# Performance work log

Measured on AMD Instinct MI355X. Metric: run time of the kernel, lower is better.

## Reference

```python
import jax, jax.numpy as jnp
import numpy as np

N = 100_000      # nodes
E = 1_600_000    # edges (avg degree 16)
C_IN, C_H, C_OUT = 32, 64, 64
G = 64           # graphs in batch


def setup_inputs() -> dict:
    key = jax.random.key(0)
    ks = jax.random.split(key, 10)
    x = jax.random.normal(ks[0], (N, C_IN), jnp.float32)
    edge_index = jax.random.randint(ks[1], (2, E), 0, N, dtype=jnp.int64)
    edge_weight = jax.random.uniform(ks[2], (E,), jnp.float32)
    batch = jnp.sort(jax.random.randint(ks[3], (N,), 0, G, dtype=jnp.int64))
    def lin(k, fan_in, fan_out):
        return jax.random.normal(k, (fan_in, fan_out), jnp.float32) / np.float32(np.sqrt(fan_in))
    W1 = lin(ks[4], C_IN, C_H)
    W2 = lin(ks[5], C_H, C_H)
    W3 = lin(ks[6], C_H, C_OUT)
    b1 = jnp.zeros((C_H,), jnp.float32)
    b2 = jnp.zeros((C_H,), jnp.float32)
    b3 = jnp.zeros((C_OUT,), jnp.float32)
    return {"x": x, "edge_weight": edge_weight, "W1": W1, "b1": b1,
            "W2": W2, "b2": b2, "W3": W3, "b3": b3,
            "edge_index": edge_index, "batch": batch}


def _gcn_norm(edge_index, edge_weight, n):
    # PyG GCNConv default: add self-loops (weight 1), symmetric D^-1/2 A D^-1/2 norm.
    loop = jnp.arange(n, dtype=edge_index.dtype)
    src = jnp.concatenate([edge_index[0], loop])
    dst = jnp.concatenate([edge_index[1], loop])
    ew = jnp.concatenate([edge_weight, jnp.ones((n,), edge_weight.dtype)])
    deg = jax.ops.segment_sum(ew, dst, num_segments=n)
    dis = jnp.where(deg > 0, jax.lax.rsqrt(deg), jnp.float32(0))
    norm = dis[src] * ew * dis[dst]
    return src, dst, norm


def _gcn_layer(h, W, b, src, dst, norm, n):
    h = h @ W                                 # [N, out]
    msg = h[src] * norm[:, None]              # gather + scale  [E+N, out]
    agg = jax.ops.segment_sum(msg, dst, num_segments=n)
    return agg + b


def reference(x, edge_weight, W1, b1, W2, b2, W3, b3, edge_index, batch):
    n = x.shape[0]
    src, dst, norm = _gcn_norm(edge_index, edge_weight, n)  # shared across layers
    h = jax.nn.silu(_gcn_layer(x, W1, b1, src, dst, norm, n))
    # Dropout(0.1) is identity in eval mode
    h = jax.nn.silu(_gcn_layer(h, W2, b2, src, dst, norm, n))
    h = jax.nn.silu(_gcn_layer(h, W3, b3, src, dst, norm, n))
    # global_mean_pool over graphs
    sums = jax.ops.segment_sum(h, batch, num_segments=G)
    counts = jax.ops.segment_sum(jnp.ones((n,), h.dtype), batch, num_segments=G)
    return sums / jnp.maximum(counts, 1)[:, None]
```

## Files before the change

kernel.cpp:

```cpp
#include <hip/hip_runtime.h>
#include <hip/hip_fp16.h>
#include <math.h>


#define NB   256
#define PBLK 1024
#define FIXP_SCALE 1048576.0f
#define FIXP_MASK  ((1ULL << 40) - 1)

__device__ __forceinline__ int lower_bound_i(const int* __restrict__ a, int n, int v) {
    int lo = 0, hi = n;
    while (lo < hi) {
        int m = (lo + hi) >> 1;
        if (a[m] < v) lo = m + 1; else hi = m;
    }
    return lo;
}

__global__ __launch_bounds__(256) void k_bhist(const int* __restrict__ dst,
                                               int* __restrict__ hcnt, int e) {
    __shared__ int hist[NB];
    int tid = threadIdx.x, blk = blockIdx.x;
    hist[tid] = 0;
    __syncthreads();
    int chunk = (e + PBLK - 1) / PBLK;
    int lo = blk * chunk, hi = min(e, lo + chunk);
    for (int i = lo + tid; i < hi; i += 256)
        atomicAdd(&hist[dst[i] >> 9], 1);
    __syncthreads();
    hcnt[tid * PBLK + blk] = hist[tid];
}

__global__ __launch_bounds__(256) void k_bscan(int* __restrict__ hcnt,
                                               int* __restrict__ btot) {
    __shared__ int s[256];
    int b = blockIdx.x, tid = threadIdx.x;
    int* row = hcnt + b * PBLK;
    int a0 = row[4 * tid], a1 = row[4 * tid + 1], a2 = row[4 * tid + 2], a3 = row[4 * tid + 3];
    int tsum = a0 + a1 + a2 + a3;
    s[tid] = tsum;
    __syncthreads();
    for (int off = 1; off < 256; off <<= 1) {
        int t = (tid >= off) ? s[tid - off] : 0;
        __syncthreads();
        s[tid] += t;
        __syncthreads();
    }
    int ex = s[tid] - tsum;
    row[4 * tid] = ex;
    row[4 * tid + 1] = ex + a0;
    row[4 * tid + 2] = ex + a0 + a1;
    row[4 * tid + 3] = ex + a0 + a1 + a2;
    if (tid == 255) btot[b] = s[255];
}

__global__ __launch_bounds__(256) void k_bbase(const int* __restrict__ btot,
                                               int* __restrict__ bbase,
                                               int* __restrict__ rowptr, int n, int e) {
    __shared__ int s[256];
    int tid = threadIdx.x;
    int v = btot[tid];
    s[tid] = v;
    __syncthreads();
    for (int off = 1; off < 256; off <<= 1) {
        int t = (tid >= off) ? s[tid - off] : 0;
        __syncthreads();
        s[tid] += t;
        __syncthreads();
    }
    bbase[tid] = s[tid] - v;
    if (tid == 255) bbase[NB] = s[255];
    if (tid == 0) rowptr[n] = e;
}

__global__ __launch_bounds__(256) void k_bpart(const int* __restrict__ src,
                                               const int* __restrict__ dst,
                                               const float* __restrict__ ew,
                                               const int* __restrict__ hcnt,
                                               const int* __restrict__ bbase,
                                               int2* __restrict__ bedge, int e) {
    __shared__ int cur[NB];
    int tid = threadIdx.x, blk = blockIdx.x;
    cur[tid] = bbase[tid] + hcnt[tid * PBLK + blk];
    __syncthreads();
    int chunk = (e + PBLK - 1) / PBLK;
    int lo = blk * chunk, hi = min(e, lo + chunk);
    for (int i = lo + tid; i < hi; i += 256) {
        int d = dst[i];
        int pos = atomicAdd(&cur[d >> 9], 1);
        bedge[pos] = make_int2(src[i] | ((d & 511) << 17), __float_as_int(ew[i]));
    }
}

__global__ __launch_bounds__(256) void k_bucket(const int2* __restrict__ bedge,
                                                const int* __restrict__ bbase,
                                                float* __restrict__ dis,
                                                int* __restrict__ rowptr,
                                                int2* __restrict__ em, int n) {
    __shared__ unsigned long long pk[512];
    __shared__ int cnt[512];
    __shared__ int scn[512];
    __shared__ float sdis[512];
    __shared__ int cur[512];
    int b = blockIdx.x, tid = threadIdx.x;
    int e0 = bbase[b], e1 = bbase[b + 1];
    pk[tid] = 0ULL; pk[tid + 256] = 0ULL;
    __syncthreads();
    for (int i = e0 + tid; i < e1; i += 256) {
        int2 v = bedge[i];
        int dlo = (v.x >> 17) & 511;
        unsigned long long p =
            (1ULL << 40) | (unsigned long long)(__int_as_float(v.y) * FIXP_SCALE);
        atomicAdd(&pk[dlo], p);
    }
    __syncthreads();
#pragma unroll
    for (int k = 0; k < 2; ++k) {
        int i = tid + k * 256;
        unsigned long long v = pk[i];
        int c = (int)(v >> 40);
        cnt[i] = c; scn[i] = c;
        sdis[i] = rsqrtf(1.0f + (float)(v & FIXP_MASK) * (1.0f / FIXP_SCALE));
    }
    __syncthreads();
    for (int off = 1; off < 512; off <<= 1) {
        int i0 = tid, i1 = tid + 256;
        int v0 = (i0 >= off) ? scn[i0 - off] : 0;
        int v1 = (i1 >= off) ? scn[i1 - off] : 0;
        __syncthreads();
        scn[i0] += v0; scn[i1] += v1;
        __syncthreads();
    }
#pragma unroll
    for (int k = 0; k < 2; ++k) {
        int i = tid + k * 256;
        int rb = e0 + scn[i] - cnt[i];
        cur[i] = rb;
        int node = (b << 9) + i;
        if (node < n) { rowptr[node] = rb; dis[node] = sdis[i]; }
    }
    __syncthreads();
    for (int i = e0 + tid; i < e1; i += 256) {
        int2 v = bedge[i];
        int dlo = (v.x >> 17) & 511;
        int pos = atomicAdd(&cur[dlo], 1);
        float w = __int_as_float(v.y) * sdis[dlo];
        em[pos] = make_int2(v.x & 0x1FFFF, __float_as_int(w));
    }
}

__global__ void k_scale(const float* __restrict__ x, const float* __restrict__ dis,
                        __half* __restrict__ hs, int total) {
    int idx = blockIdx.x * blockDim.x + threadIdx.x;
    if (idx < total) hs[idx] = __float2half(x[idx] * dis[idx >> 5]);
}

template <bool SCALE, typename OUT>
__global__ __launch_bounds__(256, 4) void k_aggmm64(const __half* __restrict__ h,
                                                    const int2* __restrict__ em,
                                                    const int* __restrict__ rowptr,
                                                    const float* __restrict__ dis,
                                                    const float* __restrict__ W,
                                                    const float* __restrict__ bias,
                                                    OUT* __restrict__ out, int n) {
    __shared__ __align__(16) float sacc[4][64];
    int lane = threadIdx.x & 63, wv = threadIdx.x >> 6;
    float w[64];
#pragma unroll
    for (int k = 0; k < 64; ++k) w[k] = W[k * 64 + lane];
    float bv = bias[lane];
    int wid = (blockIdx.x * blockDim.x + threadIdx.x) >> 6;
    int nw = (gridDim.x * blockDim.x) >> 6;
    for (int node = wid; node < n; node += nw) {
        int lo = rowptr[node], hi = rowptr[node + 1];
        int deg = hi - lo;
        float acc = dis[node] * __half2float(h[(size_t)node * 64 + lane]);
        for (int jb = 0; jb < deg; jb += 64) {
            int idx = lo + jb + lane;
            int2 me = (idx < hi) ? em[idx] : make_int2(0, 0);
            int rem = deg - jb;
#pragma unroll
            for (int g = 0; g < 4; ++g) {
                if (g * 16 < rem) {
#pragma unroll
                    for (int t = 0; t < 16; ++t) {
                        int s = __shfl(me.x, g * 16 + t, 64);
                        float ww = __int_as_float(__shfl(me.y, g * 16 + t, 64));
                        acc = fmaf(ww, __half2float(h[(size_t)s * 64 + lane]), acc);
                    }
                }
            }
        }
        sacc[wv][lane] = acc;
        float o = bv;
        const float4* s4 = (const float4*)sacc[wv];
#pragma unroll
        for (int k4 = 0; k4 < 16; ++k4) {
            float4 a4 = s4[k4];
            o = fmaf(a4.x, w[4 * k4 + 0], o);
            o = fmaf(a4.y, w[4 * k4 + 1], o);
            o = fmaf(a4.z, w[4 * k4 + 2], o);
            o = fmaf(a4.w, w[4 * k4 + 3], o);
        }
        o = o / (1.0f + __expf(-o));
        if (SCALE) o *= dis[node];
        if (sizeof(OUT) == 2) {
            ((__half*)out)[(size_t)node * 64 + lane] = __float2half(o);
        } else {
            ((float*)out)[(size_t)node * 64 + lane] = o;
        }
    }
}

__global__ __launch_bounds__(256, 4) void k_aggmm32(const __half* __restrict__ h,
                                                    const int2* __restrict__ em,
                                                    const int* __restrict__ rowptr,
                                                    const float* __restrict__ dis,
                                                    const float* __restrict__ W,
                                                    const float* __restrict__ bias,
                                                    __half* __restrict__ out, int n) {
    __shared__ __align__(16) float sacc[4][32];
    int lane = threadIdx.x & 63, wv = threadIdx.x >> 6;
    int c = lane & 31, half = lane >> 5;
    float w[32];
#pragma unroll
    for (int k = 0; k < 32; ++k) w[k] = W[k * 64 + lane];
    float bv = bias[lane];
    int wid = (blockIdx.x * blockDim.x + threadIdx.x) >> 6;
    int nw = (gridDim.x * blockDim.x) >> 6;
    for (int node = wid; node < n; node += nw) {
        int lo = rowptr[node], hi = rowptr[node + 1];
        int deg = hi - lo;
        float acc = (half == 0) ? dis[node] * __half2float(h[(size_t)node * 32 + c]) : 0.0f;
        for (int jb = 0; jb < deg; jb += 64) {
            int idx = lo + jb + lane;
            int2 me = (idx < hi) ? em[idx] : make_int2(0, 0);
            int rem = deg - jb;
#pragma unroll
            for (int g = 0; g < 4; ++g) {
                if (g * 16 < rem) {
#pragma unroll
                    for (int t = 0; t < 8; ++t) {
                        int ei = g * 16 + 2 * t + half;
                        int s = __shfl(me.x, ei, 64);
                        float ww = __int_as_float(__shfl(me.y, ei, 64));
                        acc = fmaf(ww, __half2float(h[(size_t)s * 32 + c]), acc);
                    }
                }
            }
        }
        acc += __shfl_down(acc, 32, 64);
        if (half == 0) sacc[wv][c] = acc;
        float o = bv;
        const float4* s4 = (const float4*)sacc[wv];
#pragma unroll
        for (int k4 = 0; k4 < 8; ++k4) {
            float4 a4 = s4[k4];
            o = fmaf(a4.x, w[4 * k4 + 0], o);
            o = fmaf(a4.y, w[4 * k4 + 1], o);
            o = fmaf(a4.z, w[4 * k4 + 2], o);
            o = fmaf(a4.w, w[4 * k4 + 3], o);
        }
        o = o / (1.0f + __expf(-o));
        o *= dis[node];
        out[(size_t)node * 64 + lane] = __float2half(o);
    }
}

__global__ void k_pool_partial(const float* __restrict__ h, const int* __restrict__ batch,
                               float* __restrict__ acc, int n) {
    int c = threadIdx.x & 63, r = threadIdx.x >> 6;
    int base = blockIdx.x * 128;
    int end = base + 128; if (end > n) end = n;
    float part = 0.0f;
    int cur = -1;
    for (int i = base + r; i < end; i += 4) {
        int g = batch[i];
        if (g != cur) {
            if (cur >= 0) atomicAdd(&acc[cur * 64 + c], part);
            part = 0.0f;
            cur = g;
        }
        part += h[(size_t)i * 64 + c];
    }
    if (cur >= 0) atomicAdd(&acc[cur * 64 + c], part);
}

__global__ void k_pool_final(const float* __restrict__ acc, const int* __restrict__ batch,
                             float* __restrict__ out, int n) {
    int idx = blockIdx.x * blockDim.x + threadIdx.x;
    int g = idx >> 6;
    int lo = lower_bound_i(batch, n, g);
    int hi = lower_bound_i(batch, n, g + 1);
    int cnt = hi - lo;
    out[idx] = acc[idx] / (float)(cnt > 0 ? cnt : 1);
}

extern "C" void kernel_launch(void* const* d_in, const int* in_sizes, int n_in,
                              void* d_out, int out_size, void* d_ws, size_t ws_size,
                              hipStream_t stream) {
    const float* x   = (const float*)d_in[0];
    const float* ew  = (const float*)d_in[1];
    const float* W1  = (const float*)d_in[2];
    const float* b1  = (const float*)d_in[3];
    const float* W2  = (const float*)d_in[4];
    const float* b2  = (const float*)d_in[5];
    const float* W3  = (const float*)d_in[6];
    const float* b3  = (const float*)d_in[7];
    const int*   eidx  = (const int*)d_in[8];
    const int*   batch = (const int*)d_in[9];
    float* out = (float*)d_out;

    const int E = in_sizes[1];
    const int N = in_sizes[9];
    const int G = 64;
    const int* src = eidx;
    const int* dst = eidx + E;

    char* p = (char*)d_ws;
    __half* A     = (__half*)p;                p += (size_t)N * 64 * sizeof(__half);
    __half* B     = (__half*)p;                p += (size_t)N * 64 * sizeof(__half);
    float* C      = (float*)p;                 p += (size_t)N * 64 * sizeof(float);
    float* dis    = (float*)p;                 p += (size_t)N * sizeof(float);
    int*   rowptr = (int*)p;                   p += (size_t)(N + 1) * sizeof(int);
    int*   bbase  = (int*)p;                   p += (size_t)(NB + 1) * sizeof(int);
    float* acc    = (float*)p;                 p += (size_t)G * 64 * sizeof(float);
    p = (char*)(((uintptr_t)p + 7) & ~(uintptr_t)7);
    int2*  em     = (int2*)p;

    int2* bedge = (int2*)A;
    int*  hcnt  = (int*)B;
    int*  btot  = (int*)B + NB * PBLK;

    const int BT = 256;
    const int FUSED_BLOCKS = 3125;

    k_bhist<<<PBLK, 256, 0, stream>>>(dst, hcnt, E);
    k_bscan<<<NB, 256, 0, stream>>>(hcnt, btot);
    k_bbase<<<1, 256, 0, stream>>>(btot, bbase, rowptr, N, E);
    k_bpart<<<PBLK, 256, 0, stream>>>(src, dst, ew, hcnt, bbase, bedge, E);
    k_bucket<<<NB, 256, 0, stream>>>(bedge, bbase, dis, rowptr, em, N);

    k_scale<<<(N * 32 + BT - 1) / BT, BT, 0, stream>>>(x, dis, (__half*)B, N * 32);
    k_aggmm32<<<FUSED_BLOCKS, BT, 0, stream>>>((__half*)B, em, rowptr, dis, W1, b1, A, N);

    k_aggmm64<true, __half><<<FUSED_BLOCKS, BT, 0, stream>>>(A, em, rowptr, dis, W2, b2, B, N);

    k_aggmm64<false, float><<<FUSED_BLOCKS, BT, 0, stream>>>(B, em, rowptr, dis, W3, b3, C, N);

    hipMemsetAsync(acc, 0, (size_t)G * 64 * sizeof(float), stream);
    k_pool_partial<<<(N + 127) / 128, BT, 0, stream>>>(C, batch, acc, N);
    k_pool_final<<<(G * 64) / BT, BT, 0, stream>>>(acc, batch, out, N);
}
```

Measured before the change: 386.2 us.

## Vectorize half gathers as half2 pairs and stage edge metadata in LDS

The aggregation kernels now have each lane load two channels at once as a packed half2 word. The wavefront is split into halves (64-channel) or quarters (32-channel) that handle different edges in parallel, and their partial sums are combined with shuffles. Edge indices and weights are written to per-wave shared memory and read back as int2, replacing two cross-lane shuffles per edge. The goal is more edges in flight per gather instruction and less shuffle overhead. In exchange the kernels pay for LDS traffic and extra reductions, and they rely on wave-synchronous LDS visibility with no explicit barrier.

```diff
diff --git a/kernel.cpp b/kernel.cpp
--- a/kernel.cpp
+++ b/kernel.cpp
@@ -155,6 +155,11 @@
     if (idx < total) hs[idx] = __float2half(x[idx] * dis[idx >> 5]);
 }
 
+__device__ __forceinline__ float2 cvt_pair(unsigned int u) {
+    __half2 h2 = *(__half2*)&u;
+    return __half22float2(h2);
+}
+
 template <bool SCALE, typename OUT>
 __global__ __launch_bounds__(256, 4) void k_aggmm64(const __half* __restrict__ h,
                                                     const int2* __restrict__ em,
@@ -164,7 +169,10 @@
                                                     const float* __restrict__ bias,
                                                     OUT* __restrict__ out, int n) {
     __shared__ __align__(16) float sacc[4][64];
+    __shared__ __align__(8) int2 sme[4][64];
     int lane = threadIdx.x & 63, wv = threadIdx.x >> 6;
+    int c = lane & 31, half = lane >> 5;
+    const unsigned int* h32 = (const unsigned int*)h;
     float w[64];
 #pragma unroll
     for (int k = 0; k < 64; ++k) w[k] = W[k * 64 + lane];
@@ -174,24 +182,34 @@
     for (int node = wid; node < n; node += nw) {
         int lo = rowptr[node], hi = rowptr[node + 1];
         int deg = hi - lo;
-        float acc = dis[node] * __half2float(h[(size_t)node * 64 + lane]);
+        float2 acc = make_float2(0.0f, 0.0f);
+        if (half == 0) {
+            float2 hv = cvt_pair(h32[(size_t)node * 32 + c]);
+            float di = dis[node];
+            acc.x = di * hv.x; acc.y = di * hv.y;
+        }
         for (int jb = 0; jb < deg; jb += 64) {
             int idx = lo + jb + lane;
             int2 me = (idx < hi) ? em[idx] : make_int2(0, 0);
+            sme[wv][lane] = me;
             int rem = deg - jb;
 #pragma unroll
             for (int g = 0; g < 4; ++g) {
                 if (g * 16 < rem) {
 #pragma unroll
-                    for (int t = 0; t < 16; ++t) {
-                        int s = __shfl(me.x, g * 16 + t, 64);
-                        float ww = __int_as_float(__shfl(me.y, g * 16 + t, 64));
-                        acc = fmaf(ww, __half2float(h[(size_t)s * 64 + lane]), acc);
+                    for (int t = 0; t < 8; ++t) {
+                        int2 ev = sme[wv][g * 16 + 2 * t + half];
+                        float ww = __int_as_float(ev.y);
+                        float2 hf = cvt_pair(h32[(size_t)ev.x * 32 + c]);
+                        acc.x = fmaf(ww, hf.x, acc.x);
+                        acc.y = fmaf(ww, hf.y, acc.y);
                     }
                 }
             }
         }
-        sacc[wv][lane] = acc;
+        acc.x += __shfl_down(acc.x, 32, 64);
+        acc.y += __shfl_down(acc.y, 32, 64);
+        if (half == 0) ((float2*)sacc[wv])[c] = acc;
         float o = bv;
         const float4* s4 = (const float4*)sacc[wv];
 #pragma unroll
@@ -220,8 +238,10 @@
                                                     const float* __restrict__ bias,
                                                     __half* __restrict__ out, int n) {
     __shared__ __align__(16) float sacc[4][32];
+    __shared__ __align__(8) int2 sme[4][64];
     int lane = threadIdx.x & 63, wv = threadIdx.x >> 6;
-    int c = lane & 31, half = lane >> 5;
+    int c = lane & 15, quarter = lane >> 4;
+    const unsigned int* h32 = (const unsigned int*)h;
     float w[32];
 #pragma unroll
     for (int k = 0; k < 32; ++k) w[k] = W[k * 64 + lane];
@@ -231,26 +251,36 @@
     for (int node = wid; node < n; node += nw) {
         int lo = rowptr[node], hi = rowptr[node + 1];
         int deg = hi - lo;
-        float acc = (half == 0) ? dis[node] * __half2float(h[(size_t)node * 32 + c]) : 0.0f;
+        float2 acc = make_float2(0.0f, 0.0f);
+        if (quarter == 0) {
+            float2 hv = cvt_pair(h32[(size_t)node * 16 + c]);
+            float di = dis[node];
+            acc.x = di * hv.x; acc.y = di * hv.y;
+        }
         for (int jb = 0; jb < deg; jb += 64) {
             int idx = lo + jb + lane;
             int2 me = (idx < hi) ? em[idx] : make_int2(0, 0);
+            sme[wv][lane] = me;
             int rem = deg - jb;
 #pragma unroll
             for (int g = 0; g < 4; ++g) {
                 if (g * 16 < rem) {
 #pragma unroll
-                    for (int t = 0; t < 8; ++t) {
-                        int ei = g * 16 + 2 * t + half;
-                        int s = __shfl(me.x, ei, 64);
-                        float ww = __int_as_float(__shfl(me.y, ei, 64));
-                        acc = fmaf(ww, __half2float(h[(size_t)s * 32 + c]), acc);
+                    for (int t = 0; t < 4; ++t) {
+                        int2 ev = sme[wv][g * 16 + 4 * t + quarter];
+                        float ww = __int_as_float(ev.y);
+                        float2 hf = cvt_pair(h32[(size_t)ev.x * 16 + c]);
+                        acc.x = fmaf(ww, hf.x, acc.x);
+                        acc.y = fmaf(ww, hf.y, acc.y);
                     }
                 }
             }
         }
-        acc += __shfl_down(acc, 32, 64);
-        if (half == 0) sacc[wv][c] = acc;
+        acc.x += __shfl_down(acc.x, 32, 64);
+        acc.y += __shfl_down(acc.y, 32, 64);
+        acc.x += __shfl_down(acc.x, 16, 64);
+        acc.y += __shfl_down(acc.y, 16, 64);
+        if (quarter == 0) ((float2*)sacc[wv])[c] = acc;
         float o = bv;
         const float4* s4 = (const float4*)sacc[wv];
 #pragma unroll
```

Result: faster. 349.1 us (-9.6%).

## Process two nodes per wavefront with packed half2 gathers in aggregation kernels

Applied to the files above, without the earlier changes.

Both fused aggregate+matmul kernels now handle a pair of destination nodes per wavefront. Each lane gathers a packed half2 (two channels) and the wave splits edges across halves or quarters, then reduces with shuffles. Edge metadata is staged through LDS instead of being broadcast by shuffles. W is now read from global/cache inside the matmul loop instead of being held in 64 registers, which is meant to cut register pressure and raise memory-level parallelism. The cost is extra LDS traffic, repeated W loads, and wasted work when the two nodes' degrees differ.

```diff
diff --git a/kernel.cpp b/kernel.cpp
--- a/kernel.cpp
+++ b/kernel.cpp
@@ -155,6 +155,11 @@
     if (idx < total) hs[idx] = __float2half(x[idx] * dis[idx >> 5]);
 }
 
+__device__ __forceinline__ float2 cvt_pair(unsigned int u) {
+    __half2 h2 = *(__half2*)&u;
+    return __half22float2(h2);
+}
+
 template <bool SCALE, typename OUT>
 __global__ __launch_bounds__(256, 4) void k_aggmm64(const __half* __restrict__ h,
                                                     const int2* __restrict__ em,
@@ -163,51 +168,95 @@
                                                     const float* __restrict__ W,
                                                     const float* __restrict__ bias,
                                                     OUT* __restrict__ out, int n) {
-    __shared__ __align__(16) float sacc[4][64];
+    __shared__ __align__(16) float sacc[4][2][64];
+    __shared__ __align__(8) int2 sme[4][2][64];
     int lane = threadIdx.x & 63, wv = threadIdx.x >> 6;
-    float w[64];
-#pragma unroll
-    for (int k = 0; k < 64; ++k) w[k] = W[k * 64 + lane];
+    int c = lane & 31, half = lane >> 5;
+    const unsigned int* h32 = (const unsigned int*)h;
     float bv = bias[lane];
     int wid = (blockIdx.x * blockDim.x + threadIdx.x) >> 6;
     int nw = (gridDim.x * blockDim.x) >> 6;
-    for (int node = wid; node < n; node += nw) {
-        int lo = rowptr[node], hi = rowptr[node + 1];
-        int deg = hi - lo;
-        float acc = dis[node] * __half2float(h[(size_t)node * 64 + lane]);
-        for (int jb = 0; jb < deg; jb += 64) {
-            int idx = lo + jb + lane;
-            int2 me = (idx < hi) ? em[idx] : make_int2(0, 0);
-            int rem = deg - jb;
+    int npair = (n + 1) >> 1;
+    for (int pr = wid; pr < npair; pr += nw) {
+        int n0 = 2 * pr, n1 = 2 * pr + 1;
+        bool has1 = (n1 < n);
+        int lo0 = rowptr[n0], hi0 = rowptr[n0 + 1];
+        int lo1 = has1 ? rowptr[n1] : 0, hi1 = has1 ? rowptr[n1 + 1] : 0;
+        int deg0 = hi0 - lo0, deg1 = hi1 - lo1;
+        int degm = max(deg0, deg1);
+        float2 acc0 = make_float2(0.0f, 0.0f), acc1 = make_float2(0.0f, 0.0f);
+        if (half == 0) {
+            float2 hv0 = cvt_pair(h32[(size_t)n0 * 32 + c]);
+            float d0 = dis[n0];
+            acc0.x = d0 * hv0.x; acc0.y = d0 * hv0.y;
+            if (has1) {
+                float2 hv1 = cvt_pair(h32[(size_t)n1 * 32 + c]);
+                float d1 = dis[n1];
+                acc1.x = d1 * hv1.x; acc1.y = d1 * hv1.y;
+            }
+        }
+        for (int jb = 0; jb < degm; jb += 64) {
+            int2 me0 = (jb + lane < deg0) ? em[lo0 + jb + lane] : make_int2(0, 0);
+            int2 me1 = (jb + lane < deg1) ? em[lo1 + jb + lane] : make_int2(0, 0);
+            sme[wv][0][lane] = me0;
+            sme[wv][1][lane] = me1;
+            int remm = degm - jb;
 #pragma unroll
             for (int g = 0; g < 4; ++g) {
-                if (g * 16 < rem) {
-#pragma unroll
-                    for (int t = 0; t < 16; ++t) {
-                        int s = __shfl(me.x, g * 16 + t, 64);
-                        float ww = __int_as_float(__shfl(me.y, g * 16 + t, 64));
-                        acc = fmaf(ww, __half2float(h[(size_t)s * 64 + lane]), acc);
+                if (g * 16 < remm) {
+#pragma unroll
+                    for (int t = 0; t < 8; ++t) {
+                        int ei = g * 16 + 2 * t + half;
+                        int2 e0 = sme[wv][0][ei];
+                        int2 e1 = sme[wv][1][ei];
+                        float w0 = __int_as_float(e0.y);
+                        float w1 = __int_as_float(e1.y);
+                        float2 f0 = cvt_pair(h32[(size_t)e0.x * 32 + c]);
+                        float2 f1 = cvt_pair(h32[(size_t)e1.x * 32 + c]);
+                        acc0.x = fmaf(w0, f0.x, acc0.x);
+                        acc0.y = fmaf(w0, f0.y, acc0.y);
+                        acc1.x = fmaf(w1, f1.x, acc1.x);
+                        acc1.y = fmaf(w1, f1.y, acc1.y);
                     }
                 }
             }
         }
-        sacc[wv][lane] = acc;
-        float o = bv;
-        const float4* s4 = (const float4*)sacc[wv];
+        acc0.x += __shfl_down(acc0.x, 32, 64);
+        acc0.y += __shfl_down(acc0.y, 32, 64);
+        acc1.x += __shfl_down(acc1.x, 32, 64);
+        acc1.y += __shfl_down(acc1.y, 32, 64);
+        if (half == 0) {
+            ((float2*)sacc[wv][0])[c] = acc0;
+            ((float2*)sacc[wv][1])[c] = acc1;
+        }
+        float o0 = bv, o1 = bv;
+        const float4* s40 = (const float4*)sacc[wv][0];
+        const float4* s41 = (const float4*)sacc[wv][1];
 #pragma unroll
         for (int k4 = 0; k4 < 16; ++k4) {
-            float4 a4 = s4[k4];
-            o = fmaf(a4.x, w[4 * k4 + 0], o);
-            o = fmaf(a4.y, w[4 * k4 + 1], o);
-            o = fmaf(a4.z, w[4 * k4 + 2], o);
-            o = fmaf(a4.w, w[4 * k4 + 3], o);
-        }
-        o = o / (1.0f + __expf(-o));
-        if (SCALE) o *= dis[node];
+            float w0 = W[(4 * k4 + 0) * 64 + lane];
+            float w1 = W[(4 * k4 + 1) * 64 + lane];
+            float w2 = W[(4 * k4 + 2) * 64 + lane];
+            float w3 = W[(4 * k4 + 3) * 64 + lane];
+            float4 a0 = s40[k4];
+            float4 a1 = s41[k4];
+            o0 = fmaf(a0.x, w0, o0); o1 = fmaf(a1.x, w0, o1);
+            o0 = fmaf(a0.y, w1, o0); o1 = fmaf(a1.y, w1, o1);
+            o0 = fmaf(a0.z, w2, o0); o1 = fmaf(a1.z, w2, o1);
+            o0 = fmaf(a0.w, w3, o0); o1 = fmaf(a1.w, w3, o1);
+        }
+        o0 = o0 / (1.0f + __expf(-o0));
+        o1 = o1 / (1.0f + __expf(-o1));
+        if (SCALE) {
+            o0 *= dis[n0];
+            if (has1) o1 *= dis[n1];
+        }
         if (sizeof(OUT) == 2) {
-            ((__half*)out)[(size_t)node * 64 + lane] = __float2half(o);
+            ((__half*)out)[(size_t)n0 * 64 + lane] = __float2half(o0);
+            if (has1) ((__half*)out)[(size_t)n1 * 64 + lane] = __float2half(o1);
         } else {
-            ((float*)out)[(size_t)node * 64 + lane] = o;
+            ((float*)out)[(size_t)n0 * 64 + lane] = o0;
+            if (has1) ((float*)out)[(size_t)n1 * 64 + lane] = o1;
         }
     }
 }
@@ -219,51 +268,95 @@
                                                     const float* __restrict__ W,
                                                     const float* __restrict__ bias,
                                                     __half* __restrict__ out, int n) {
-    __shared__ __align__(16) float sacc[4][32];
+    __shared__ __align__(16) float sacc[4][2][32];
+    __shared__ __align__(8) int2 sme[4][2][64];
     int lane = threadIdx.x & 63, wv = threadIdx.x >> 6;
-    int c = lane & 31, half = lane >> 5;
-    float w[32];
-#pragma unroll
-    for (int k = 0; k < 32; ++k) w[k] = W[k * 64 + lane];
+    int c = lane & 15, quarter = lane >> 4;
+    const unsigned int* h32 = (const unsigned int*)h;
     float bv = bias[lane];
     int wid = (blockIdx.x * blockDim.x + threadIdx.x) >> 6;
     int nw = (gridDim.x * blockDim.x) >> 6;
-    for (int node = wid; node < n; node += nw) {
-        int lo = rowptr[node], hi = rowptr[node + 1];
-        int deg = hi - lo;
-        float acc = (half == 0) ? dis[node] * __half2float(h[(size_t)node * 32 + c]) : 0.0f;
-        for (int jb = 0; jb < deg; jb += 64) {
-            int idx = lo + jb + lane;
-            int2 me = (idx < hi) ? em[idx] : make_int2(0, 0);
-            int rem = deg - jb;
+    int npair = (n + 1) >> 1;
+    for (int pr = wid; pr < npair; pr += nw) {
+        int n0 = 2 * pr, n1 = 2 * pr + 1;
+        bool has1 = (n1 < n);
+        int lo0 = rowptr[n0], hi0 = rowptr[n0 + 1];
+        int lo1 = has1 ? rowptr[n1] : 0, hi1 = has1 ? rowptr[n1 + 1] : 0;
+        int deg0 = hi0 - lo0, deg1 = hi1 - lo1;
+        int degm = max(deg0, deg1);
+        float2 acc0 = make_float2(0.0f, 0.0f), acc1 = make_float2(0.0f, 0.0f);
+        if (quarter == 0) {
+            float2 hv0 = cvt_pair(h32[(size_t)n0 * 16 + c]);
+            float d0 = dis[n0];
+            acc0.x = d0 * hv0.x; acc0.y = d0 * hv0.y;
+            if (has1) {
+                float2 hv1 = cvt_pair(h32[(size_t)n1 * 16 + c]);
+                float d1 = dis[n1];
+                acc1.x = d1 * hv1.x; acc1.y = d1 * hv1.y;
+            }
+        }
+        for (int jb = 0; jb < degm; jb += 64) {
+            int2 me0 = (jb + lane < deg0) ? em[lo0 + jb + lane] : make_int2(0, 0);
+            int2 me1 = (jb + lane < deg1) ? em[lo1 + jb + lane] : make_int2(0, 0);
+            sme[wv][0][lane] = me0;
+            sme[wv][1][lane] = me1;
+            int remm = degm - jb;
 #pragma unroll
             for (int g = 0; g < 4; ++g) {
-                if (g * 16 < rem) {
-#pragma unroll
-                    for (int t = 0; t < 8; ++t) {
-                        int ei = g * 16 + 2 * t + half;
-                        int s = __shfl(me.x, ei, 64);
-                        float ww = __int_as_float(__shfl(me.y, ei, 64));
-                        acc = fmaf(ww, __half2float(h[(size_t)s * 32 + c]), acc);
+                if (g * 16 < remm) {
+#pragma unroll
+                    for (int t = 0; t < 4; ++t) {
+                        int ei = g * 16 + 4 * t + quarter;
+                        int2 e0 = sme[wv][0][ei];
+                        int2 e1 = sme[wv][1][ei];
+                        float w0 = __int_as_float(e0.y);
+                        float w1 = __int_as_float(e1.y);
+                        float2 f0 = cvt_pair(h32[(size_t)e0.x * 16 + c]);
+                        float2 f1 = cvt_pair(h32[(size_t)e1.x * 16 + c]);
+                        acc0.x = fmaf(w0, f0.x, acc0.x);
+                        acc0.y = fmaf(w0, f0.y, acc0.y);
+                        acc1.x = fmaf(w1, f1.x, acc1.x);
+                        acc1.y = fmaf(w1, f1.y, acc1.y);
                     }
                 }
             }
         }
-        acc += __shfl_down(acc, 32, 64);
-        if (half == 0) sacc[wv][c] = acc;
-        float o = bv;
-        const float4* s4 = (const float4*)sacc[wv];
+        acc0.x += __shfl_down(acc0.x, 32, 64);
+        acc0.y += __shfl_down(acc0.y, 32, 64);
+        acc1.x += __shfl_down(acc1.x, 32, 64);
+        acc1.y += __shfl_down(acc1.y, 32, 64);
+        acc0.x += __shfl_down(acc0.x, 16, 64);
+        acc0.y += __shfl_down(acc0.y, 16, 64);
+        acc1.x += __shfl_down(acc1.x, 16, 64);
+        acc1.y += __shfl_down(acc1.y, 16, 64);
+        if (quarter == 0) {
+            ((float2*)sacc[wv][0])[c] = acc0;
+            ((float2*)sacc[wv][1])[c] = acc1;
+        }
+        float o0 = bv, o1 = bv;
+        const float4* s40 = (const float4*)sacc[wv][0];
+        const float4* s41 = (const float4*)sacc[wv][1];
 #pragma unroll
         for (int k4 = 0; k4 < 8; ++k4) {
-            float4 a4 = s4[k4];
-            o = fmaf(a4.x, w[4 * k4 + 0], o);
-            o = fmaf(a4.y, w[4 * k4 + 1], o);
-            o = fmaf(a4.z, w[4 * k4 + 2], o);
-            o = fmaf(a4.w, w[4 * k4 + 3], o);
-        }
-        o = o / (1.0f + __expf(-o));
-        o *= dis[node];
-        out[(size_t)node * 64 + lane] = __float2half(o);
+            float w0 = W[(4 * k4 + 0) * 64 + lane];
+            float w1 = W[(4 * k4 + 1) * 64 + lane];
+            float w2 = W[(4 * k4 + 2) * 64 + lane];
+            float w3 = W[(4 * k4 + 3) * 64 + lane];
+            float4 a0 = s40[k4];
+            float4 a1 = s41[k4];
+            o0 = fmaf(a0.x, w0, o0); o1 = fmaf(a1.x, w0, o1);
+            o0 = fmaf(a0.y, w1, o0); o1 = fmaf(a1.y, w1, o1);
+            o0 = fmaf(a0.z, w2, o0); o1 = fmaf(a1.z, w2, o1);
+            o0 = fmaf(a0.w, w3, o0); o1 = fmaf(a1.w, w3, o1);
+        }
+        o0 = o0 / (1.0f + __expf(-o0));
+        o1 = o1 / (1.0f + __expf(-o1));
+        o0 *= dis[n0];
+        out[(size_t)n0 * 64 + lane] = __float2half(o0);
+        if (has1) {
+            o1 *= dis[n1];
+            out[(size_t)n1 * 64 + lane] = __float2half(o1);
+        }
     }
 }
 
```

After: 402.4 us. 1.04x slower.
